# Kernel tuning notes

Measured on AMD Instinct MI355X. Metric: run time of the kernel, lower is better.

The kernel has to match this reference:

```python
import jax, jax.numpy as jnp
import numpy as np

DIM = 384
HEADS = 8
RATES = (0.5, 0.75)  # sparse_rates
EPS = 1e-12  # torch F.normalize default eps


def _dwconv3x3(x, w):
    # depthwise 3x3, padding=1; w: [3*dim, 1, 3, 3]
    return jax.lax.conv_general_dilated(
        x, w, window_strides=(1, 1), padding=((1, 1), (1, 1)),
        feature_group_count=w.shape[0],
        dimension_numbers=('NCHW', 'OIHW', 'NCHW'))


def setup_inputs() -> dict:
    key = jax.random.key(0)
    ks = jax.random.split(key, 5)
    dim = DIM
    x = jax.random.normal(ks[0], (4, dim, 128, 128), jnp.float32)
    qkv_w = jax.random.normal(ks[1], (3 * dim, dim), jnp.float32) * 0.05   # 1x1 conv
    dw_w = jax.random.normal(ks[2], (3 * dim, 1, 3, 3), jnp.float32) * 0.1  # depthwise 3x3
    proj_w = jax.random.normal(ks[3], (dim, dim), jnp.float32) * 0.05       # 1x1 conv
    temperature = jnp.ones((HEADS, 1, 1), jnp.float32)
    attns = jnp.full((len(RATES),), 0.2, jnp.float32)
    return {"x": x, "qkv_w": qkv_w, "dw_w": dw_w, "proj_w": proj_w,
            "temperature": temperature, "attns": attns}


def reference(x, qkv_w, dw_w, proj_w, temperature, attns) -> jnp.ndarray:
    b, c, h, w = x.shape
    qkv = jnp.einsum('bchw,oc->bohw', x, qkv_w)  # 1x1 conv, no bias
    qkv = _dwconv3x3(qkv, dw_w)
    q, k, v = jnp.split(qkv, 3, axis=1)

    def heads(t):  # b (head c) h w -> b head c (h w)
        return t.reshape(b, HEADS, c // HEADS, h * w)

    q, k, v = heads(q), heads(k), heads(v)
    q = q / jnp.maximum(jnp.linalg.norm(q, axis=-1, keepdims=True), EPS)
    k = k / jnp.maximum(jnp.linalg.norm(k, axis=-1, keepdims=True), EPS)
    C = q.shape[2]
    attn = jnp.einsum('bhcn,bhdn->bhcd', q, k) * temperature  # [b, head, C, C]

    out = jnp.zeros_like(v)  # [b, head, C, HW]
    for i, rate in enumerate(RATES):
        kk = int(C * rate)
        _, idx = jax.lax.top_k(attn, kk)                      # [b, head, C, kk]
        mask = jax.nn.one_hot(idx, C, dtype=attn.dtype).sum(-2) > 0  # scatter 1s
        attn = jnp.where(mask, attn, -jnp.inf)
        attn = jax.nn.softmax(attn, axis=-1)  # NOTE: original reuses softmaxed attn next iter
        out = out + jnp.einsum('bhcd,bhdn->bhcn', attn, v) * attns[i]

    out = out.reshape(b, c, h, w)  # b head c (hw) -> b (head c) h w
    return jnp.einsum('bchw,oc->bohw', out, proj_w)
```

## Files before the change

### kernel.cpp

```cpp
#include <hip/hip_runtime.h>
#include <math.h>

#define HW     16384
#define WIDTH  128
#define CDIM   384
#define QKVC   1152
#define HEADS  8
#define CH     48
#define NSPLIT 32
#define GK     384

typedef unsigned short u16;
typedef short bf16x8 __attribute__((ext_vector_type(8)));
typedef u16 u16x8 __attribute__((ext_vector_type(8)));
typedef float f32x4 __attribute__((ext_vector_type(4)));

__device__ __forceinline__ void split2(float x, u16& h, u16& l) {
    union { float f; unsigned u; } a, b, c;
    a.f = x;
    unsigned hu = (a.u + 0x7fffu + ((a.u >> 16) & 1u)) & 0xffff0000u;
    b.u = hu;
    h = (u16)(hu >> 16);
    c.f = x - b.f;
    l = (u16)((c.u + 0x7fffu + ((c.u >> 16) & 1u)) >> 16);
}

__device__ __forceinline__ void gload16(const void* g, void* l) {
    __builtin_amdgcn_global_load_lds((const __attribute__((address_space(1))) unsigned int*)g,
                                     (__attribute__((address_space(3))) unsigned int*)l, 16, 0, 0);
}

__global__ __launch_bounds__(256)
void mfma_gemm(const u16* __restrict__ Ah, const u16* __restrict__ Al,
               const u16* __restrict__ Bh, const u16* __restrict__ Bl,
               float* __restrict__ C, int nmb,
               long abs_, long bbs, long cbs)
{
    extern __shared__ char smem[];
    const int tot = gridDim.x * gridDim.y;
    const int per = tot >> 3;
    const int fl  = blockIdx.x + gridDim.x * blockIdx.y;
    const int f2  = (fl & 7) * per + (fl >> 3);
    const int nblk = f2 / nmb, mblk = f2 % nmb;
    const int b = blockIdx.z;
    Ah += (long)b * abs_; Al += (long)b * abs_;
    Bh += (long)b * bbs;  Bl += (long)b * bbs;
    C  += (long)b * cbs;
    const int m0 = mblk * 128, n0 = nblk * 128;

    const int tid  = threadIdx.x;
    const int wave = tid >> 6, lane = tid & 63;
    const int lr = lane & 15, lg = lane >> 4;
    const int wm = wave >> 1, wn = wave & 1;

    const int srow = tid >> 2;
    const int kc   = tid & 3;
    const int sw   = kc ^ ((srow >> 1) & 3);

    f32x4 acc[4][4];
#pragma unroll
    for (int i = 0; i < 4; ++i)
#pragma unroll
        for (int j = 0; j < 4; ++j) acc[i][j] = (f32x4){0.f, 0.f, 0.f, 0.f};

#define STAGE(bs, kt) do { char* LL = smem + (bs) * 32768;                          \
        const long ko = (long)(kt) * 32 + sw * 8;                                   \
        gload16(Ah + (long)(m0 + srow) * GK      + ko, LL + tid * 16);              \
        gload16(Ah + (long)(m0 + 64 + srow) * GK + ko, LL + 4096  + tid * 16);      \
        gload16(Al + (long)(m0 + srow) * GK      + ko, LL + 8192  + tid * 16);      \
        gload16(Al + (long)(m0 + 64 + srow) * GK + ko, LL + 12288 + tid * 16);      \
        gload16(Bh + (long)(n0 + srow) * GK      + ko, LL + 16384 + tid * 16);      \
        gload16(Bh + (long)(n0 + 64 + srow) * GK + ko, LL + 20480 + tid * 16);      \
        gload16(Bl + (long)(n0 + srow) * GK      + ko, LL + 24576 + tid * 16);      \
        gload16(Bl + (long)(n0 + 64 + srow) * GK + ko, LL + 28672 + tid * 16);      \
    } while (0)

    STAGE(0, 0);
    __syncthreads();
#pragma unroll
    for (int kt = 0; kt < 12; ++kt) {
        if (kt + 1 < 12) STAGE((kt + 1) & 1, kt + 1);

        const char* L = smem + (kt & 1) * 32768;
        bf16x8 af[4][2], bf[4][2];
#pragma unroll
        for (int mi = 0; mi < 4; ++mi) {
            int r = wm * 64 + mi * 16 + lr;
            int off = r * 64 + (((lg ^ (r >> 1)) & 3) << 4);
            af[mi][0] = *(const bf16x8*)(L + off);
            af[mi][1] = *(const bf16x8*)(L + 8192 + off);
        }
#pragma unroll
        for (int ni = 0; ni < 4; ++ni) {
            int r = wn * 64 + ni * 16 + lr;
            int off = r * 64 + (((lg ^ (r >> 1)) & 3) << 4);
            bf[ni][0] = *(const bf16x8*)(L + 16384 + off);
            bf[ni][1] = *(const bf16x8*)(L + 24576 + off);
        }

        __builtin_amdgcn_s_setprio(1);
#pragma unroll
        for (int mi = 0; mi < 4; ++mi)
#pragma unroll
            for (int ni = 0; ni < 4; ++ni) {
                acc[mi][ni] = __builtin_amdgcn_mfma_f32_16x16x32_bf16(af[mi][0], bf[ni][0], acc[mi][ni], 0, 0, 0);
                acc[mi][ni] = __builtin_amdgcn_mfma_f32_16x16x32_bf16(af[mi][0], bf[ni][1], acc[mi][ni], 0, 0, 0);
                acc[mi][ni] = __builtin_amdgcn_mfma_f32_16x16x32_bf16(af[mi][1], bf[ni][0], acc[mi][ni], 0, 0, 0);
            }
        __builtin_amdgcn_s_setprio(0);
        __syncthreads();
    }
#undef STAGE

#pragma unroll
    for (int mi = 0; mi < 4; ++mi)
#pragma unroll
        for (int ni = 0; ni < 4; ++ni) {
            int row = m0 + wm * 64 + mi * 16 + lg * 4;
            int col = n0 + wn * 64 + ni * 16 + lr;
            float* cp = C + (long)row * HW + col;
            cp[0]          = acc[mi][ni][0];
            cp[(long)HW]   = acc[mi][ni][1];
            cp[2L * HW]    = acc[mi][ni][2];
            cp[3L * HW]    = acc[mi][ni][3];
        }
}

__global__ __launch_bounds__(256)
void convT_kernel(const float* __restrict__ in, u16* __restrict__ oh, u16* __restrict__ ol,
                  long ibs, long obs)
{
    const int b = blockIdx.z;
    in += (long)b * ibs; oh += (long)b * obs; ol += (long)b * obs;
    __shared__ float t[32][33];
    const int p0 = blockIdx.x * 32, c0 = blockIdx.y * 32;
    const int ty = threadIdx.x >> 5, tx = threadIdx.x & 31;
#pragma unroll
    for (int it = 0; it < 4; ++it) {
        int c = ty + it * 8;
        t[c][tx] = in[(long)(c0 + c) * HW + p0 + tx];
    }
    __syncthreads();
    const int cp = threadIdx.x & 15;
    const int py = threadIdx.x >> 4;
#pragma unroll
    for (int half = 0; half < 2; ++half) {
        int p = py + half * 16;
        u16 h0, l0, h1, l1;
        split2(t[2 * cp][p], h0, l0);
        split2(t[2 * cp + 1][p], h1, l1);
        long o = (long)(p0 + p) * CDIM + c0 + 2 * cp;
        *(ushort2*)&oh[o] = (ushort2){h0, h1};
        *(ushort2*)&ol[o] = (ushort2){l0, l1};
    }
}

__global__ __launch_bounds__(256)
void convA_kernel(const float* __restrict__ in, u16* __restrict__ oh, u16* __restrict__ ol, int n)
{
    int i = blockIdx.x * 256 + threadIdx.x;
    if (i < n) split2(in[i], oh[i], ol[i]);
}

__global__ __launch_bounds__(256)
void dwconv_kernel(const float* __restrict__ in, const float* __restrict__ w,
                   float* __restrict__ out)
{
    const long base = (long)blockIdx.y * QKVC * HW;
    const int idx = blockIdx.x * 256 + threadIdx.x;
    const int ch = idx >> 11;
    const int wi = idx & 2047;
    const int y = wi >> 4, x0 = (wi & 15) * 8;
    const float* wp = w + ch * 9;
    const float* ip = in + base + (long)ch * HW;
    float o[8] = {0.f, 0.f, 0.f, 0.f, 0.f, 0.f, 0.f, 0.f};
#pragma unroll
    for (int dy = -1; dy <= 1; ++dy) {
        int yy = y + dy;
        if ((unsigned)yy >= 128u) continue;
        const float* rp = ip + yy * WIDTH + x0;
        float4 a  = *(const float4*)rp;
        float4 bq = *(const float4*)(rp + 4);
        float v[10] = { (x0 > 0) ? rp[-1] : 0.f,
                        a.x, a.y, a.z, a.w, bq.x, bq.y, bq.z, bq.w,
                        (x0 < 120) ? rp[8] : 0.f };
        float w0 = wp[(dy + 1) * 3], w1 = wp[(dy + 1) * 3 + 1], w2 = wp[(dy + 1) * 3 + 2];
#pragma unroll
        for (int j = 0; j < 8; ++j)
            o[j] = fmaf(w0, v[j], fmaf(w1, v[j + 1], fmaf(w2, v[j + 2], o[j])));
    }
    float* op = out + base + (long)ch * HW + y * WIDTH + x0;
    *(float4*)op       = (float4){o[0], o[1], o[2], o[3]};
    *(float4*)(op + 4) = (float4){o[4], o[5], o[6], o[7]};
}

__global__ __launch_bounds__(256)
void dwconv_vT_kernel(const float* __restrict__ in, const float* __restrict__ w,
                      u16* __restrict__ oh, u16* __restrict__ ol, long ibs, long obs)
{
    const int b  = blockIdx.z;
    const int cg = blockIdx.y;
    const int p0 = blockIdx.x * 64;
    const int y  = p0 >> 7, xh = p0 & 127;
    __shared__ unsigned pk[64][97];

    const int tid = threadIdx.x;
    const int seg = tid & 7;
    const int chl = tid >> 3;
    const int x0  = xh + seg * 8;
#pragma unroll
    for (int cp = 0; cp < 3; ++cp) {
        const int cl = cp * 32 + chl;
        const int c  = cg * 96 + cl;
        const float* ip = in + (long)b * ibs + (long)(768 + c) * HW;
        const float* wp = w + (768 + c) * 9;
        float o[8] = {0.f, 0.f, 0.f, 0.f, 0.f, 0.f, 0.f, 0.f};
#pragma unroll
        for (int dy = -1; dy <= 1; ++dy) {
            int yy = y + dy;
            if ((unsigned)yy >= 128u) continue;
            const float* rp = ip + yy * WIDTH + x0;
            float4 a  = *(const float4*)rp;
            float4 bq = *(const float4*)(rp + 4);
            float v[10] = { (x0 > 0) ? rp[-1] : 0.f,
                            a.x, a.y, a.z, a.w, bq.x, bq.y, bq.z, bq.w,
                            (x0 < 120) ? rp[8] : 0.f };
            float w0 = wp[(dy + 1) * 3], w1 = wp[(dy + 1) * 3 + 1], w2 = wp[(dy + 1) * 3 + 2];
#pragma unroll
            for (int j = 0; j < 8; ++j)
                o[j] = fmaf(w0, v[j], fmaf(w1, v[j + 1], fmaf(w2, v[j + 2], o[j])));
        }
#pragma unroll
        for (int j = 0; j < 8; ++j) {
            u16 hh, ll;
            split2(o[j], hh, ll);
            pk[seg * 8 + j][cl] = ((unsigned)hh << 16) | ll;
        }
    }
    __syncthreads();
    const int px = tid >> 2, qt = tid & 3;
    u16 hs[24], ls[24];
#pragma unroll
    for (int j = 0; j < 24; ++j) {
        unsigned v = pk[px][qt * 24 + j];
        hs[j] = (u16)(v >> 16);
        ls[j] = (u16)(v & 0xffffu);
    }
    u16* ph = oh + (long)b * obs + (long)(p0 + px) * CDIM + cg * 96 + qt * 24;
    u16* pl = ol + (long)b * obs + (long)(p0 + px) * CDIM + cg * 96 + qt * 24;
#pragma unroll
    for (int j = 0; j < 3; ++j) {
        *(u16x8*)(ph + j * 8) = *(const u16x8*)&hs[j * 8];
        *(u16x8*)(pl + j * 8) = *(const u16x8*)&ls[j * 8];
    }
}

__global__ __launch_bounds__(256)
void attn_partial_kernel(const float* __restrict__ dw, float* __restrict__ part,
                         float* __restrict__ part2, long ps, long p2s)
{
    const int split = blockIdx.x, h = blockIdx.y, b = blockIdx.z;
    const int n0 = split * (HW / NSPLIT);
    const float* qbase = dw + ((long)b * QKVC + h * CH) * HW;
    const float* kbase = dw + ((long)b * QKVC + CDIM + h * CH) * HW;
    __shared__ float qs[48][68];
    __shared__ float ks[48][68];
    const int tid = threadIdx.x;
    const int tr = tid >> 4, tc = tid & 15;
    const int c0 = tr * 3, d0 = tc * 3;
    float acc[3][3] = {{0.f}};
    float qss[3] = {0.f, 0.f, 0.f}, kss[3] = {0.f, 0.f, 0.f};
    const int cA = tid >> 4;
    const int nq = (tid & 15) * 4;

#define DOT4(I, J, Q, K) do {                               \
        acc[I][J] = fmaf((Q).x, (K).x, acc[I][J]);          \
        acc[I][J] = fmaf((Q).y, (K).y, acc[I][J]);          \
        acc[I][J] = fmaf((Q).z, (K).z, acc[I][J]);          \
        acc[I][J] = fmaf((Q).w, (K).w, acc[I][J]);          \
    } while (0)

    for (int ns = 0; ns < HW / NSPLIT; ns += 64) {
        __syncthreads();
#pragma unroll
        for (int t = 0; t < 3; ++t) {
            int c = cA + t * 16;
            float4 qv = *(const float4*)(qbase + (long)c * HW + n0 + ns + nq);
            float4 kv = *(const float4*)(kbase + (long)c * HW + n0 + ns + nq);
            *(float4*)&qs[c][nq] = qv;
            *(float4*)&ks[c][nq] = kv;
            qss[t] += qv.x * qv.x + qv.y * qv.y + qv.z * qv.z + qv.w * qv.w;
            kss[t] += kv.x * kv.x + kv.y * kv.y + kv.z * kv.z + kv.w * kv.w;
        }
        __syncthreads();
#pragma unroll 4
        for (int nn = 0; nn < 64; nn += 4) {
            float4 qa = *(const float4*)&qs[c0 + 0][nn];
            float4 qb = *(const float4*)&qs[c0 + 1][nn];
            float4 qc = *(const float4*)&qs[c0 + 2][nn];
            float4 ka = *(const float4*)&ks[d0 + 0][nn];
            float4 kb = *(const float4*)&ks[d0 + 1][nn];
            float4 kc = *(const float4*)&ks[d0 + 2][nn];
            DOT4(0, 0, qa, ka); DOT4(0, 1, qa, kb); DOT4(0, 2, qa, kc);
            DOT4(1, 0, qb, ka); DOT4(1, 1, qb, kb); DOT4(1, 2, qb, kc);
            DOT4(2, 0, qc, ka); DOT4(2, 1, qc, kb); DOT4(2, 2, qc, kc);
        }
    }
#undef DOT4
#pragma unroll
    for (int m = 1; m < 16; m <<= 1) {
#pragma unroll
        for (int t = 0; t < 3; ++t) {
            qss[t] += __shfl_xor(qss[t], m);
            kss[t] += __shfl_xor(kss[t], m);
        }
    }
    if ((tid & 15) == 0) {
        float* p2 = part2 + (long)b * p2s + ((long)h * NSPLIT + split) * 96;
#pragma unroll
        for (int t = 0; t < 3; ++t) {
            p2[cA + t * 16]      = qss[t];
            p2[48 + cA + t * 16] = kss[t];
        }
    }
    float* po = part + (long)b * ps + ((long)h * NSPLIT + split) * (CH * CH);
#pragma unroll
    for (int i = 0; i < 3; ++i)
#pragma unroll
        for (int j = 0; j < 3; ++j)
            po[(c0 + i) * CH + d0 + j] = acc[i][j];
}

__global__ __launch_bounds__(256)
void attn_reduce_kernel(const float* __restrict__ part, const float* __restrict__ part2,
                        const float* __restrict__ temp, float* __restrict__ attn,
                        long ps, long p2s, long as_)
{
    const int seg = blockIdx.x, h = blockIdx.y, b = blockIdx.z;
    const float* pp = part + (long)b * ps + (long)h * NSPLIT * (CH * CH);
    const float* p2 = part2 + (long)b * p2s + (long)h * NSPLIT * 96;
    __shared__ float sinv[96];
    if (threadIdx.x < 96) {
        float s = 0.f;
        for (int sp = 0; sp < NSPLIT; ++sp) s += p2[sp * 96 + threadIdx.x];
        sinv[threadIdx.x] = 1.f / fmaxf(sqrtf(s), 1e-12f);
    }
    __syncthreads();
    const float t = temp[h];
    const int idx = seg * 256 + threadIdx.x;
    const int c = idx / CH, d = idx % CH;
    float s = 0.f;
    for (int sp = 0; sp < NSPLIT; ++sp) s += pp[sp * (CH * CH) + idx];
    attn[(long)b * as_ + (long)h * (CH * CH) + idx] = s * sinv[c] * sinv[48 + d] * t;
}

__global__ __launch_bounds__(256)
void maskw_kernel(const float* __restrict__ attn, const float* __restrict__ attns,
                  float* __restrict__ W, long as_, long ws_)
{
    const int h = blockIdx.y, b = blockIdx.z;
    const int wave = threadIdx.x >> 6, lane = threadIdx.x & 63;
    const int r = blockIdx.x * 4 + wave;
    const float* ap = attn + (long)b * as_ + (long)h * (CH * CH) + (long)r * CH;
    float a = (lane < CH) ? ap[lane] : -3.4e38f;

    int rank = 0;
#pragma unroll
    for (int j = 0; j < CH; ++j) {
        float aj = __shfl(a, j);
        rank += (aj > a) || (aj == a && j < lane);
    }
    const bool keep = (lane < CH) && (rank < 24);
    float m = keep ? a : -3.4e38f;
#pragma unroll
    for (int o = 32; o > 0; o >>= 1) m = fmaxf(m, __shfl_xor(m, o));
    float e = keep ? expf(a - m) : 0.f;
    float s = e;
#pragma unroll
    for (int o = 32; o > 0; o >>= 1) s += __shfl_xor(s, o);
    const float A1 = e / s;

    int rank2 = 0;
#pragma unroll
    for (int j = 0; j < CH; ++j) {
        float aj = __shfl(A1, j);
        rank2 += (aj > A1) || (aj == A1 && j < lane);
    }
    const bool keep2 = (lane < CH) && (rank2 < 36);
    float m2 = keep2 ? A1 : -3.4e38f;
#pragma unroll
    for (int o = 32; o > 0; o >>= 1) m2 = fmaxf(m2, __shfl_xor(m2, o));
    float e2 = keep2 ? expf(A1 - m2) : 0.f;
    float s2 = e2;
#pragma unroll
    for (int o = 32; o > 0; o >>= 1) s2 += __shfl_xor(s2, o);

    if (lane < CH)
        W[(long)b * ws_ + (long)h * (CH * CH) + (long)r * CH + lane] =
            attns[0] * A1 + attns[1] * (e2 / s2);
}

__global__ __launch_bounds__(256)
void mbuild_kernel(const float* __restrict__ P, const float* __restrict__ W,
                   u16* __restrict__ Mh, u16* __restrict__ Ml, long ws_, long ms)
{
    const int b = blockIdx.y;
    const int idx = blockIdx.x * 256 + threadIdx.x;
    const int o = idx / CDIM, col = idx % CDIM;
    const int h = col / CH, d = col % CH;
    const float* wp = W + (long)b * ws_ + (long)h * (CH * CH) + d;
    const float* pp = P + (long)o * CDIM + h * CH;
    float s = 0.f;
#pragma unroll
    for (int c = 0; c < CH; ++c) s = fmaf(pp[c], wp[c * CH], s);
    u16 hh, ll;
    split2(s, hh, ll);
    Mh[(long)b * ms + idx] = hh;
    Ml[(long)b * ms + idx] = ll;
}

extern "C" void kernel_launch(void* const* d_in, const int* in_sizes, int n_in,
                              void* d_out, int out_size, void* d_ws, size_t ws_size,
                              hipStream_t stream)
{
    const float* x      = (const float*)d_in[0];
    const float* qkv_w  = (const float*)d_in[1];
    const float* dw_w   = (const float*)d_in[2];
    const float* proj_w = (const float*)d_in[3];
    const float* temp   = (const float*)d_in[4];
    const float* attns  = (const float*)d_in[5];
    float* out = (float*)d_out;

    const size_t perbB = (size_t)QKVC * HW * 4;
    auto need = [&](int nb) -> size_t {
        return (size_t)nb * 2 * perbB + 4u * QKVC * CDIM + 4096;
    };
    int NB = 4;
    while (NB > 1 && need(NB) > ws_size) NB >>= 1;

    const long fstride = (long)(perbB / 4);
    const long ustride = (long)(perbB / 2);

    const size_t PART_B  = 27u << 20;
    const size_t PART2_B = (29u << 20) + (512u << 10);
    const size_t ATT_B   = 30u << 20;
    const size_t WM_B    = 31u << 20;
    const size_t MH_B    = 32u << 20;
    const size_t ML_B    = 33u << 20;

    char* buf1 = (char*)d_ws;
    char* buf2 = buf1 + (size_t)NB * perbB;
    u16* Ah = (u16*)(buf2 + (size_t)NB * perbB);
    u16* Al = Ah + (size_t)QKVC * CDIM;

    convA_kernel<<<dim3((QKVC * CDIM + 255) / 256), 256, 0, stream>>>(qkv_w, Ah, Al, QKVC * CDIM);

    for (int b0 = 0; b0 < 4; b0 += NB) {
        const int nb = NB;
        float* pre = (float*)buf1;
        float* dwb = (float*)buf2;
        u16* xt_h = (u16*)buf2;                u16* xt_l = xt_h + (size_t)HW * CDIM;
        u16* vt_h = (u16*)(dwb + (size_t)768 * HW);
        u16* vt_l = vt_h + (size_t)CDIM * HW;
        float* part  = (float*)(buf1 + PART_B);
        float* part2 = (float*)(buf1 + PART2_B);
        float* attn  = (float*)(buf1 + ATT_B);
        float* Wm    = (float*)(buf1 + WM_B);
        u16* Mh = (u16*)(buf1 + MH_B);
        u16* Ml = (u16*)(buf1 + ML_B);

        convT_kernel<<<dim3(HW / 32, CDIM / 32, nb), 256, 0, stream>>>(
            x + (size_t)b0 * CDIM * HW, xt_h, xt_l, (long)CDIM * HW, ustride);
        mfma_gemm<<<dim3(HW / 128, QKVC / 128, nb), 256, 65536, stream>>>(
            Ah, Al, xt_h, xt_l, pre, QKVC / 128, 0L, ustride, fstride);
        dwconv_kernel<<<dim3(768 * HW / 8 / 256, nb), 256, 0, stream>>>(pre, dw_w, dwb);
        dwconv_vT_kernel<<<dim3(HW / 64, 4, nb), 256, 0, stream>>>(pre, dw_w, vt_h, vt_l,
                                                                   fstride, ustride);
        attn_partial_kernel<<<dim3(NSPLIT, HEADS, nb), 256, 0, stream>>>(dwb, part, part2,
                                                                         fstride, fstride);
        attn_reduce_kernel<<<dim3(9, HEADS, nb), 256, 0, stream>>>(part, part2, temp, attn,
                                                                   fstride, fstride, fstride);
        maskw_kernel<<<dim3(12, HEADS, nb), 256, 0, stream>>>(attn, attns, Wm, fstride, fstride);
        mbuild_kernel<<<dim3(CDIM * CDIM / 256, nb), 256, 0, stream>>>(proj_w, Wm, Mh, Ml,
                                                                       fstride, ustride);
        mfma_gemm<<<dim3(HW / 128, CDIM / 128, nb), 256, 65536, stream>>>(
            Mh, Ml, vt_h, vt_l, out + (size_t)b0 * CDIM * HW, CDIM / 128,
            ustride, ustride, (long)CDIM * HW);
    }
}
```

Measured before the change: 620.0 us.

## Fuse attention reduce, top-k mask softmax and projection build into one kernel

Replaces three small launches (partial-sum reduction, top-k masked softmax weights, and proj×W matrix build) with a single per-(head,batch) kernel that keeps the 48x48 attention matrix in shared memory. This removes two kernel launches and the global round trips for the attn and W buffers. In exchange the grid shrinks to only 32 blocks, so the reduction and the M-build run with far less parallelism than before.

```diff
diff --git a/kernel.cpp b/kernel.cpp
--- a/kernel.cpp
+++ b/kernel.cpp
@@ -332,91 +332,85 @@
 }
 
 __global__ __launch_bounds__(256)
-void attn_reduce_kernel(const float* __restrict__ part, const float* __restrict__ part2,
-                        const float* __restrict__ temp, float* __restrict__ attn,
-                        long ps, long p2s, long as_)
-{
-    const int seg = blockIdx.x, h = blockIdx.y, b = blockIdx.z;
+void tail_kernel(const float* __restrict__ part, const float* __restrict__ part2,
+                 const float* __restrict__ temp, const float* __restrict__ attns,
+                 const float* __restrict__ P, u16* __restrict__ Mh, u16* __restrict__ Ml,
+                 long ps, long p2s, long ms)
+{
+    const int h = blockIdx.x, b = blockIdx.y;
+    const int tid = threadIdx.x;
+    __shared__ float sW[48][49];
+    __shared__ float sinv[96];
+
+    if (tid < 96) {
+        const float* p2 = part2 + (long)b * p2s + (long)h * NSPLIT * 96;
+        float s = 0.f;
+        for (int sp = 0; sp < NSPLIT; ++sp) s += p2[sp * 96 + tid];
+        sinv[tid] = 1.f / fmaxf(sqrtf(s), 1e-12f);
+    }
+    __syncthreads();
+
+    const float t = temp[h];
     const float* pp = part + (long)b * ps + (long)h * NSPLIT * (CH * CH);
-    const float* p2 = part2 + (long)b * p2s + (long)h * NSPLIT * 96;
-    __shared__ float sinv[96];
-    if (threadIdx.x < 96) {
+    for (int idx = tid; idx < CH * CH; idx += 256) {
+        int c = idx / CH, d = idx % CH;
         float s = 0.f;
-        for (int sp = 0; sp < NSPLIT; ++sp) s += p2[sp * 96 + threadIdx.x];
-        sinv[threadIdx.x] = 1.f / fmaxf(sqrtf(s), 1e-12f);
-    }
-    __syncthreads();
-    const float t = temp[h];
-    const int idx = seg * 256 + threadIdx.x;
-    const int c = idx / CH, d = idx % CH;
-    float s = 0.f;
-    for (int sp = 0; sp < NSPLIT; ++sp) s += pp[sp * (CH * CH) + idx];
-    attn[(long)b * as_ + (long)h * (CH * CH) + idx] = s * sinv[c] * sinv[48 + d] * t;
-}
-
-__global__ __launch_bounds__(256)
-void maskw_kernel(const float* __restrict__ attn, const float* __restrict__ attns,
-                  float* __restrict__ W, long as_, long ws_)
-{
-    const int h = blockIdx.y, b = blockIdx.z;
-    const int wave = threadIdx.x >> 6, lane = threadIdx.x & 63;
-    const int r = blockIdx.x * 4 + wave;
-    const float* ap = attn + (long)b * as_ + (long)h * (CH * CH) + (long)r * CH;
-    float a = (lane < CH) ? ap[lane] : -3.4e38f;
-
-    int rank = 0;
-#pragma unroll
-    for (int j = 0; j < CH; ++j) {
-        float aj = __shfl(a, j);
-        rank += (aj > a) || (aj == a && j < lane);
-    }
-    const bool keep = (lane < CH) && (rank < 24);
-    float m = keep ? a : -3.4e38f;
-#pragma unroll
-    for (int o = 32; o > 0; o >>= 1) m = fmaxf(m, __shfl_xor(m, o));
-    float e = keep ? expf(a - m) : 0.f;
-    float s = e;
-#pragma unroll
-    for (int o = 32; o > 0; o >>= 1) s += __shfl_xor(s, o);
-    const float A1 = e / s;
-
-    int rank2 = 0;
-#pragma unroll
-    for (int j = 0; j < CH; ++j) {
-        float aj = __shfl(A1, j);
-        rank2 += (aj > A1) || (aj == A1 && j < lane);
-    }
-    const bool keep2 = (lane < CH) && (rank2 < 36);
-    float m2 = keep2 ? A1 : -3.4e38f;
-#pragma unroll
-    for (int o = 32; o > 0; o >>= 1) m2 = fmaxf(m2, __shfl_xor(m2, o));
-    float e2 = keep2 ? expf(A1 - m2) : 0.f;
-    float s2 = e2;
-#pragma unroll
-    for (int o = 32; o > 0; o >>= 1) s2 += __shfl_xor(s2, o);
-
-    if (lane < CH)
-        W[(long)b * ws_ + (long)h * (CH * CH) + (long)r * CH + lane] =
-            attns[0] * A1 + attns[1] * (e2 / s2);
-}
-
-__global__ __launch_bounds__(256)
-void mbuild_kernel(const float* __restrict__ P, const float* __restrict__ W,
-                   u16* __restrict__ Mh, u16* __restrict__ Ml, long ws_, long ms)
-{
-    const int b = blockIdx.y;
-    const int idx = blockIdx.x * 256 + threadIdx.x;
-    const int o = idx / CDIM, col = idx % CDIM;
-    const int h = col / CH, d = col % CH;
-    const float* wp = W + (long)b * ws_ + (long)h * (CH * CH) + d;
-    const float* pp = P + (long)o * CDIM + h * CH;
-    float s = 0.f;
-#pragma unroll
-    for (int c = 0; c < CH; ++c) s = fmaf(pp[c], wp[c * CH], s);
-    u16 hh, ll;
-    split2(s, hh, ll);
-    Mh[(long)b * ms + idx] = hh;
-    Ml[(long)b * ms + idx] = ll;
+        for (int sp = 0; sp < NSPLIT; ++sp) s += pp[sp * (CH * CH) + idx];
+        sW[c][d] = s * sinv[c] * sinv[48 + d] * t;
+    }
+    __syncthreads();
+
+    const int wv = tid >> 6, lane = tid & 63;
+    const float w0 = attns[0], w1 = attns[1];
+    for (int r = wv; r < CH; r += 4) {
+        float a = (lane < CH) ? sW[r][lane] : -3.4e38f;
+        int rank = 0;
+#pragma unroll
+        for (int j = 0; j < CH; ++j) {
+            float aj = __shfl(a, j);
+            rank += (aj > a) || (aj == a && j < lane);
+        }
+        const bool keep = (lane < CH) && (rank < 24);
+        float m = keep ? a : -3.4e38f;
+#pragma unroll
+        for (int o = 32; o > 0; o >>= 1) m = fmaxf(m, __shfl_xor(m, o));
+        float e = keep ? expf(a - m) : 0.f;
+        float s = e;
+#pragma unroll
+        for (int o = 32; o > 0; o >>= 1) s += __shfl_xor(s, o);
+        const float A1 = e / s;
+
+        int rank2 = 0;
+#pragma unroll
+        for (int j = 0; j < CH; ++j) {
+            float aj = __shfl(A1, j);
+            rank2 += (aj > A1) || (aj == A1 && j < lane);
+        }
+        const bool keep2 = (lane < CH) && (rank2 < 36);
+        float m2 = keep2 ? A1 : -3.4e38f;
+#pragma unroll
+        for (int o = 32; o > 0; o >>= 1) m2 = fmaxf(m2, __shfl_xor(m2, o));
+        float e2 = keep2 ? expf(A1 - m2) : 0.f;
+        float s2 = e2;
+#pragma unroll
+        for (int o = 32; o > 0; o >>= 1) s2 += __shfl_xor(s2, o);
+
+        if (lane < CH) sW[r][lane] = w0 * A1 + w1 * (e2 / s2);
+    }
+    __syncthreads();
+
+    for (int idx = tid; idx < CDIM * CH; idx += 256) {
+        int o = idx / CH, d = idx % CH;
+        const float* pr = P + (long)o * CDIM + h * CH;
+        float s = 0.f;
+#pragma unroll
+        for (int c = 0; c < CH; ++c) s = fmaf(pr[c], sW[c][d], s);
+        u16 hh, ll;
+        split2(s, hh, ll);
+        long off = (long)b * ms + (long)o * CDIM + h * CH + d;
+        Mh[off] = hh;
+        Ml[off] = ll;
+    }
 }
 
 extern "C" void kernel_launch(void* const* d_in, const int* in_sizes, int n_in,
@@ -443,8 +437,6 @@
 
     const size_t PART_B  = 27u << 20;
     const size_t PART2_B = (29u << 20) + (512u << 10);
-    const size_t ATT_B   = 30u << 20;
-    const size_t WM_B    = 31u << 20;
     const size_t MH_B    = 32u << 20;
     const size_t ML_B    = 33u << 20;
 
@@ -464,8 +456,6 @@
         u16* vt_l = vt_h + (size_t)CDIM * HW;
         float* part  = (float*)(buf1 + PART_B);
         float* part2 = (float*)(buf1 + PART2_B);
-        float* attn  = (float*)(buf1 + ATT_B);
-        float* Wm    = (float*)(buf1 + WM_B);
         u16* Mh = (u16*)(buf1 + MH_B);
         u16* Ml = (u16*)(buf1 + ML_B);
 
@@ -478,11 +468,8 @@
                                                                    fstride, ustride);
         attn_partial_kernel<<<dim3(NSPLIT, HEADS, nb), 256, 0, stream>>>(dwb, part, part2,
                                                                          fstride, fstride);
-        attn_reduce_kernel<<<dim3(9, HEADS, nb), 256, 0, stream>>>(part, part2, temp, attn,
-                                                                   fstride, fstride, fstride);
-        maskw_kernel<<<dim3(12, HEADS, nb), 256, 0, stream>>>(attn, attns, Wm, fstride, fstride);
-        mbuild_kernel<<<dim3(CDIM * CDIM / 256, nb), 256, 0, stream>>>(proj_w, Wm, Mh, Ml,
-                                                                       fstride, ustride);
+        tail_kernel<<<dim3(HEADS, nb), 256, 0, stream>>>(part, part2, temp, attns, proj_w,
+                                                         Mh, Ml, fstride, fstride, ustride);
         mfma_gemm<<<dim3(HW / 128, CDIM / 128, nb), 256, 65536, stream>>>(
             Mh, Ml, vt_h, vt_l, out + (size_t)b0 * CDIM * HW, CDIM / 128,
             ustride, ustride, (long)CDIM * HW);
```

After: 793.0 us. +27.9%, slower.
